# Kernel optimization log

Measured on AMD Instinct MI355X. Metric: run time of the kernel, lower is better.

## Reference

```python
import jax, jax.numpy as jnp
import numpy as np

B, L, H = 8192, 64, 128
DEPTH = 3
EPS = 1e-5


def setup_inputs() -> dict:
    key = jax.random.key(0)
    ks = jax.random.split(key, 1 + 6)
    hidden_states = jax.random.normal(ks[0], (B, L, H), dtype=jnp.float32)
    # stacked per-layer params: Linear(H,H) -> LayerNorm(H) -> ReLU -> Linear(H, H//2)
    s1 = 1.0 / np.sqrt(H)
    W1 = jax.random.uniform(ks[1], (DEPTH, H, H), jnp.float32, -s1, s1)
    b1 = jax.random.uniform(ks[2], (DEPTH, H), jnp.float32, -s1, s1)
    gamma = jnp.ones((DEPTH, H), jnp.float32)
    beta = jnp.zeros((DEPTH, H), jnp.float32)
    W2 = jax.random.uniform(ks[3], (DEPTH, H, H // 2), jnp.float32, -s1, s1)
    b2 = jax.random.uniform(ks[4], (DEPTH, H // 2), jnp.float32, -s1, s1)
    return {
        "hidden_states": hidden_states,
        "W1": W1, "b1": b1, "gamma": gamma, "beta": beta,
        "W2": W2, "b2": b2,
        "lengths": L,
    }


def _layernorm(x, g, b):
    mu = jnp.mean(x, axis=-1, keepdims=True)
    var = jnp.mean(jnp.square(x - mu), axis=-1, keepdims=True)
    return (x - mu) * jax.lax.rsqrt(var + EPS) * g + b


def reference(hidden_states, W1, b1, gamma, beta, W2, b2, lengths):
    # hidden_states: [B, L, H]; max(lengths) == L
    x = hidden_states
    for i in range(DEPTH):
        h = jnp.einsum('blh,hk->blk', x, W1[i]) + b1[i]          # [B, L, H]
        h = jax.nn.relu(_layernorm(h, gamma[i], beta[i]))
        x1 = jnp.einsum('blh,hk->blk', h, W2[i]) + b2[i]          # [B, L, H//2]
        x2 = jnp.max(x1, axis=1, keepdims=True)                   # max-pool over seq
        x2 = jnp.broadcast_to(x2, x1.shape)                       # repeat to L
        x = jnp.concatenate([x1, x2], axis=2)                     # [B, L, H]
    return jnp.max(x, axis=1)                                     # [B, H]
```

## Files before the change

### kernel.cpp

```cpp
#include <hip/hip_runtime.h>

#define NB 8192
#define NL 64
#define NH 128

typedef __bf16 bf16x8 __attribute__((ext_vector_type(8)));
typedef float f32x4 __attribute__((ext_vector_type(4)));
typedef float f32x2 __attribute__((ext_vector_type(2)));
typedef unsigned short ushort8 __attribute__((ext_vector_type(8)));

__device__ __host__ __forceinline__ int p2l(int p) {
  return (p & ~31) + ((p & 1) << 4) + ((p & 31) >> 1);
}
__device__ __host__ __forceinline__ int pi2(int p) {
  return (p & 1) ? 64 + (p >> 1) : (p >> 1);
}

__device__ __forceinline__ unsigned pk2(float lo, float hi) {
  union { __bf16 b[2]; unsigned u; } t;
  t.b[0] = (__bf16)lo; t.b[1] = (__bf16)hi;
  return t.u;
}

__global__ __launch_bounds__(256) void repack_w(const float* __restrict__ W1,
                                                const float* __restrict__ W2,
                                                const float* __restrict__ gamma,
                                                const float* __restrict__ beta,
                                                unsigned short* __restrict__ wp1,
                                                unsigned short* __restrict__ wp2,
                                                float* __restrict__ gbt) {
  int t = blockIdx.x * 256 + threadIdx.x;
  int lane = t & 63, g = t >> 6;
  if (g < 96) {
    int layer = g >> 5, rem = g & 31, nt = rem >> 2, ks = rem & 3;
    int n = nt * 16 + (lane & 15);
    int kb = ks * 32 + (lane >> 4) * 8;
    ushort8 v;
#pragma unroll
    for (int r = 0; r < 8; ++r) {
      int k = kb + r;
      int srck = (layer == 0) ? k : pi2(k);
      union { __bf16 b; unsigned short u; } c;
      c.b = (__bf16)W1[(layer * 128 + srck) * 128 + n];
      v[r] = c.u;
    }
    *reinterpret_cast<ushort8*>(wp1 + ((size_t)g * 64 + lane) * 8) = v;
  } else if (g < 144) {
    int g2 = g - 96;
    int layer = g2 >> 4, rem = g2 & 15, nt = rem >> 2, ks = rem & 3;
    int n = nt * 16 + (lane & 15);
    int kb = ks * 32 + (lane >> 4) * 8;
    ushort8 v;
#pragma unroll
    for (int r = 0; r < 8; ++r) {
      union { __bf16 b; unsigned short u; } c;
      c.b = (__bf16)W2[(layer * 128 + p2l(kb + r)) * 64 + n];
      v[r] = c.u;
    }
    *reinterpret_cast<ushort8*>(wp2 + ((size_t)g2 * 64 + lane) * 8) = v;
  } else if (g < 150) {
    int g2 = g - 144;
    int layer = g2 >> 1, param = g2 & 1;
    const float* src = (param == 0 ? gamma : beta) + layer * 128;
    float* dst = gbt + layer * 288 + param * 144;
    int p0 = lane * 2;
#pragma unroll
    for (int u = 0; u < 2; ++u) {
      int p = p0 + u;
      dst[(p >> 5) * 36 + (p & 31)] = src[p2l(p)];
    }
  }
}

__global__ __launch_bounds__(256) void fused_mlp(
    const float* __restrict__ hidden,
    const float* __restrict__ b1,
    const float* __restrict__ b2,
    const unsigned short* __restrict__ wp1u,
    const unsigned short* __restrict__ wp2u,
    const float* __restrict__ gbt,
    float* __restrict__ out) {
  __shared__ __align__(16) unsigned short xAu[NL * NH];
  __shared__ __align__(16) unsigned short xBu[NL * NH];
  __shared__ __align__(16) float gbuf[864];

  const int tid = threadIdx.x;
  const int wave = tid >> 6, lane = tid & 63;
  const int ci = lane & 15, lg = lane >> 4;
  char* xA = reinterpret_cast<char*>(xAu);
  char* xB = reinterpret_cast<char*>(xBu);

  const int abase = ci * 256;
  const int axor = ci << 4;

  if (tid < 96) {
#pragma unroll
    for (int u = 0; u < 9; ++u) gbuf[tid * 9 + u] = gbt[tid * 9 + u];
  }

  const float* src = hidden + (size_t)blockIdx.x * (NL * NH);
#pragma unroll
  for (int i = 0; i < 4; ++i) {
    int f = i * 256 + tid;
    int row = f >> 4;
    int cb = (f & 15) * 16;
    const float4* p = reinterpret_cast<const float4*>(src + f * 8);
    float4 a = p[0], bq = p[1];
    bf16x8 v;
    v[0] = (__bf16)a.x;  v[1] = (__bf16)a.y;  v[2] = (__bf16)a.z;  v[3] = (__bf16)a.w;
    v[4] = (__bf16)bq.x; v[5] = (__bf16)bq.y; v[6] = (__bf16)bq.z; v[7] = (__bf16)bq.w;
    *reinterpret_cast<bf16x8*>(xA + row * 256 + (cb ^ ((row & 15) << 4))) = v;
  }
  __syncthreads();

  for (int layer = 0; layer < 3; ++layer) {
    const unsigned short* wl1 = wp1u + (size_t)layer * 16384;
    const float bv0 = b1[layer * 128 + wave * 32 + ci];
    const float bv1 = b1[layer * 128 + wave * 32 + 16 + ci];
    const int dby = (wave * 16 + ci) * 4;

    f32x4 acc[4][2];
#pragma unroll
    for (int mt = 0; mt < 4; ++mt) {
      acc[mt][0] = f32x4{bv0, bv0, bv0, bv0};
      acc[mt][1] = f32x4{bv1, bv1, bv1, bv1};
    }
#pragma unroll
    for (int ks = 0; ks < 4; ++ks) {
      bf16x8 bf0 = *reinterpret_cast<const bf16x8*>(
          wl1 + (((wave * 2 + 0) * 4 + ks) * 64 + lane) * 8);
      bf16x8 bf1 = *reinterpret_cast<const bf16x8*>(
          wl1 + (((wave * 2 + 1) * 4 + ks) * 64 + lane) * 8);
      int cbx = ((ks * 64 + lg * 16) ^ axor) + abase;
#pragma unroll
      for (int mt = 0; mt < 4; ++mt) {
        bf16x8 af = *reinterpret_cast<const bf16x8*>(xA + mt * 4096 + cbx);
        acc[mt][0] = __builtin_amdgcn_mfma_f32_16x16x32_bf16(af, bf0, acc[mt][0], 0, 0, 0);
        acc[mt][1] = __builtin_amdgcn_mfma_f32_16x16x32_bf16(af, bf1, acc[mt][1], 0, 0, 0);
      }
    }
#pragma unroll
    for (int mt = 0; mt < 4; ++mt)
#pragma unroll
      for (int r = 0; r < 4; ++r) {
        int row = mt * 16 + lg * 4 + r;
        *reinterpret_cast<unsigned*>(
            xB + row * 256 + (dby ^ ((lg * 4 + r) << 4))) =
            pk2(acc[mt][0][r], acc[mt][1][r]);
      }
    __syncthreads();

    {
      const int row = wave * 16 + (lane >> 2);
      const int q = lane & 3;
      const int rb = row * 256, rx = (lane >> 2) << 4;
      bf16x8 h0 = *reinterpret_cast<const bf16x8*>(xB + rb + ((q * 64 + 0) ^ rx));
      bf16x8 h1 = *reinterpret_cast<const bf16x8*>(xB + rb + ((q * 64 + 16) ^ rx));
      bf16x8 h2 = *reinterpret_cast<const bf16x8*>(xB + rb + ((q * 64 + 32) ^ rx));
      bf16x8 h3 = *reinterpret_cast<const bf16x8*>(xB + rb + ((q * 64 + 48) ^ rx));
      f32x2 f[16];
#pragma unroll
      for (int cch = 0; cch < 4; ++cch) {
        bf16x8 hv = (cch == 0) ? h0 : (cch == 1) ? h1 : (cch == 2) ? h2 : h3;
#pragma unroll
        for (int j2 = 0; j2 < 4; ++j2)
          f[cch * 4 + j2] = f32x2{(float)hv[j2 * 2], (float)hv[j2 * 2 + 1]};
      }
      f32x2 s2 = {0.f, 0.f}, q2 = {0.f, 0.f};
#pragma unroll
      for (int i = 0; i < 16; ++i) { s2 += f[i]; q2 += f[i] * f[i]; }
      float s = s2.x + s2.y, sq = q2.x + q2.y;
      s += __shfl_xor(s, 1);  sq += __shfl_xor(sq, 1);
      s += __shfl_xor(s, 2);  sq += __shfl_xor(sq, 2);
      float mu = s * (1.f / 128.f);
      float var = sq * (1.f / 128.f) - mu * mu;
      float rs = rsqrtf(var + 1e-5f);
      const f32x2* gl = reinterpret_cast<const f32x2*>(gbuf + layer * 288 + q * 36);
      const f32x2* bl = reinterpret_cast<const f32x2*>(gbuf + layer * 288 + 144 + q * 36);
#pragma unroll
      for (int cch = 0; cch < 4; ++cch) {
        union { unsigned u[4]; bf16x8 v; } yy;
#pragma unroll
        for (int j2 = 0; j2 < 4; ++j2) {
          int i = cch * 4 + j2;
          f32x2 a2 = gl[i] * rs;
          f32x2 c2 = bl[i] - a2 * mu;
          f32x2 y2 = f[i] * a2 + c2;
          yy.u[j2] = pk2(fmaxf(y2.x, 0.f), fmaxf(y2.y, 0.f));
        }
        *reinterpret_cast<bf16x8*>(xB + rb + ((q * 64 + cch * 16) ^ rx)) = yy.v;
      }
    }
    __syncthreads();

    const unsigned short* wl2 = wp2u + (size_t)layer * 8192;
    f32x4 acc2[4];
    {
      float b2v = b2[layer * 64 + wave * 16 + ci];
#pragma unroll
      for (int mt = 0; mt < 4; ++mt) acc2[mt] = f32x4{b2v, b2v, b2v, b2v};
    }
#pragma unroll
    for (int ks = 0; ks < 4; ++ks) {
      bf16x8 bfr = *reinterpret_cast<const bf16x8*>(
          wl2 + ((wave * 4 + ks) * 64 + lane) * 8);
      int cbx = ((ks * 64 + lg * 16) ^ axor) + abase;
#pragma unroll
      for (int mt = 0; mt < 4; ++mt) {
        bf16x8 af = *reinterpret_cast<const bf16x8*>(xB + mt * 4096 + cbx);
        acc2[mt] = __builtin_amdgcn_mfma_f32_16x16x32_bf16(af, bfr, acc2[mt], 0, 0, 0);
      }
    }

    float mm;
    {
      float m = -3.0e38f;
#pragma unroll
      for (int mt = 0; mt < 4; ++mt)
#pragma unroll
        for (int r = 0; r < 4; ++r) m = fmaxf(m, acc2[mt][r]);
      m = fmaxf(m, __shfl_xor(m, 16));
      m = fmaxf(m, __shfl_xor(m, 32));
      mm = m;
    }

    if (layer < 2) {
#pragma unroll
      for (int mt = 0; mt < 4; ++mt)
#pragma unroll
        for (int r = 0; r < 4; ++r) {
          int row = mt * 16 + lg * 4 + r;
          *reinterpret_cast<unsigned*>(
              xA + row * 256 + (dby ^ ((lg * 4 + r) << 4))) =
              pk2(acc2[mt][r], mm);
        }
      __syncthreads();
    } else {
      if (lg == 0) {
        size_t o = (size_t)blockIdx.x * 128 + wave * 16 + ci;
        out[o] = mm;
        out[o + 64] = mm;
      }
    }
  }
}

extern "C" void kernel_launch(void* const* d_in, const int* in_sizes, int n_in,
                              void* d_out, int out_size, void* d_ws, size_t ws_size,
                              hipStream_t stream) {
  const float* hidden = (const float*)d_in[0];
  const float* W1 = (const float*)d_in[1];
  const float* b1 = (const float*)d_in[2];
  const float* gamma = (const float*)d_in[3];
  const float* beta = (const float*)d_in[4];
  const float* W2 = (const float*)d_in[5];
  const float* b2 = (const float*)d_in[6];
  (void)in_sizes; (void)n_in; (void)out_size; (void)ws_size;

  unsigned short* wp1 = (unsigned short*)d_ws;
  unsigned short* wp2 = wp1 + 3 * 8 * 4 * 64 * 8;
  float* gbt = (float*)(wp2 + 3 * 4 * 4 * 64 * 8);
  float* out = (float*)d_out;

  repack_w<<<38, 256, 0, stream>>>(W1, W2, gamma, beta, wp1, wp2, gbt);
  fused_mlp<<<NB, 256, 0, stream>>>(hidden, b1, b2, wp1, wp2, gbt, out);
}
```

Before: 144.1 us.

## Process two batch rows per block with software-pipelined interleaved stages

Each block now handles two sequences, using the two shared-memory buffers as per-sequence activations, and interleaves the GEMM, LayerNorm and pack stages of the two so one sequence's MFMA work overlaps the other's LDS and VALU work. The grid is halved. This aims to hide barrier stalls and the serial stage dependencies inside a single sequence, and to reuse the weight-fragment loads across two sequences. In exchange it raises register pressure from doubled accumulators, which may reduce occupancy, and leaves half as many blocks to fill the GPU.

```diff
diff --git a/kernel.cpp b/kernel.cpp
--- a/kernel.cpp
+++ b/kernel.cpp
@@ -92,34 +92,42 @@
 
   const int abase = ci * 256;
   const int axor = ci << 4;
+  const int dby = (wave * 16 + ci) * 4;
 
   if (tid < 96) {
 #pragma unroll
     for (int u = 0; u < 9; ++u) gbuf[tid * 9 + u] = gbt[tid * 9 + u];
   }
 
-  const float* src = hidden + (size_t)blockIdx.x * (NL * NH);
-#pragma unroll
-  for (int i = 0; i < 4; ++i) {
-    int f = i * 256 + tid;
-    int row = f >> 4;
-    int cb = (f & 15) * 16;
-    const float4* p = reinterpret_cast<const float4*>(src + f * 8);
-    float4 a = p[0], bq = p[1];
-    bf16x8 v;
-    v[0] = (__bf16)a.x;  v[1] = (__bf16)a.y;  v[2] = (__bf16)a.z;  v[3] = (__bf16)a.w;
-    v[4] = (__bf16)bq.x; v[5] = (__bf16)bq.y; v[6] = (__bf16)bq.z; v[7] = (__bf16)bq.w;
-    *reinterpret_cast<bf16x8*>(xA + row * 256 + (cb ^ ((row & 15) << 4))) = v;
+  {
+    const float* srcA = hidden + (size_t)(2 * blockIdx.x) * (NL * NH);
+#pragma unroll
+    for (int rr = 0; rr < 2; ++rr) {
+      const float* src = srcA + rr * (NL * NH);
+      char* xr = rr ? xB : xA;
+#pragma unroll
+      for (int i = 0; i < 4; ++i) {
+        int f = i * 256 + tid;
+        int row = f >> 4;
+        int cb = (f & 15) * 16;
+        const float4* p = reinterpret_cast<const float4*>(src + f * 8);
+        float4 a = p[0], bq = p[1];
+        bf16x8 v;
+        v[0] = (__bf16)a.x;  v[1] = (__bf16)a.y;  v[2] = (__bf16)a.z;  v[3] = (__bf16)a.w;
+        v[4] = (__bf16)bq.x; v[5] = (__bf16)bq.y; v[6] = (__bf16)bq.z; v[7] = (__bf16)bq.w;
+        *reinterpret_cast<bf16x8*>(xr + row * 256 + (cb ^ ((row & 15) << 4))) = v;
+      }
+    }
   }
   __syncthreads();
 
-  for (int layer = 0; layer < 3; ++layer) {
-    const unsigned short* wl1 = wp1u + (size_t)layer * 16384;
-    const float bv0 = b1[layer * 128 + wave * 32 + ci];
-    const float bv1 = b1[layer * 128 + wave * 32 + 16 + ci];
-    const int dby = (wave * 16 + ci) * 4;
-
-    f32x4 acc[4][2];
+  f32x4 accA[4][2], accB[4][2], acc2A[4], acc2B[4];
+  float mmA = 0.f, mmB = 0.f;
+
+  auto G1 = [&](const char* xR, f32x4 (&acc)[4][2], int l) {
+    const unsigned short* wl1 = wp1u + (size_t)l * 16384;
+    float bv0 = b1[l * 128 + wave * 32 + ci];
+    float bv1 = b1[l * 128 + wave * 32 + 16 + ci];
 #pragma unroll
     for (int mt = 0; mt < 4; ++mt) {
       acc[mt][0] = f32x4{bv0, bv0, bv0, bv0};
@@ -134,72 +142,72 @@
       int cbx = ((ks * 64 + lg * 16) ^ axor) + abase;
 #pragma unroll
       for (int mt = 0; mt < 4; ++mt) {
-        bf16x8 af = *reinterpret_cast<const bf16x8*>(xA + mt * 4096 + cbx);
+        bf16x8 af = *reinterpret_cast<const bf16x8*>(xR + mt * 4096 + cbx);
         acc[mt][0] = __builtin_amdgcn_mfma_f32_16x16x32_bf16(af, bf0, acc[mt][0], 0, 0, 0);
         acc[mt][1] = __builtin_amdgcn_mfma_f32_16x16x32_bf16(af, bf1, acc[mt][1], 0, 0, 0);
       }
     }
+  };
+
+  auto WH = [&](char* xR, f32x4 (&acc)[4][2]) {
 #pragma unroll
     for (int mt = 0; mt < 4; ++mt)
 #pragma unroll
       for (int r = 0; r < 4; ++r) {
         int row = mt * 16 + lg * 4 + r;
         *reinterpret_cast<unsigned*>(
-            xB + row * 256 + (dby ^ ((lg * 4 + r) << 4))) =
+            xR + row * 256 + (dby ^ ((lg * 4 + r) << 4))) =
             pk2(acc[mt][0][r], acc[mt][1][r]);
       }
-    __syncthreads();
-
-    {
-      const int row = wave * 16 + (lane >> 2);
-      const int q = lane & 3;
-      const int rb = row * 256, rx = (lane >> 2) << 4;
-      bf16x8 h0 = *reinterpret_cast<const bf16x8*>(xB + rb + ((q * 64 + 0) ^ rx));
-      bf16x8 h1 = *reinterpret_cast<const bf16x8*>(xB + rb + ((q * 64 + 16) ^ rx));
-      bf16x8 h2 = *reinterpret_cast<const bf16x8*>(xB + rb + ((q * 64 + 32) ^ rx));
-      bf16x8 h3 = *reinterpret_cast<const bf16x8*>(xB + rb + ((q * 64 + 48) ^ rx));
-      f32x2 f[16];
-#pragma unroll
-      for (int cch = 0; cch < 4; ++cch) {
-        bf16x8 hv = (cch == 0) ? h0 : (cch == 1) ? h1 : (cch == 2) ? h2 : h3;
-#pragma unroll
-        for (int j2 = 0; j2 < 4; ++j2)
-          f[cch * 4 + j2] = f32x2{(float)hv[j2 * 2], (float)hv[j2 * 2 + 1]};
-      }
-      f32x2 s2 = {0.f, 0.f}, q2 = {0.f, 0.f};
-#pragma unroll
-      for (int i = 0; i < 16; ++i) { s2 += f[i]; q2 += f[i] * f[i]; }
-      float s = s2.x + s2.y, sq = q2.x + q2.y;
-      s += __shfl_xor(s, 1);  sq += __shfl_xor(sq, 1);
-      s += __shfl_xor(s, 2);  sq += __shfl_xor(sq, 2);
-      float mu = s * (1.f / 128.f);
-      float var = sq * (1.f / 128.f) - mu * mu;
-      float rs = rsqrtf(var + 1e-5f);
-      const f32x2* gl = reinterpret_cast<const f32x2*>(gbuf + layer * 288 + q * 36);
-      const f32x2* bl = reinterpret_cast<const f32x2*>(gbuf + layer * 288 + 144 + q * 36);
-#pragma unroll
-      for (int cch = 0; cch < 4; ++cch) {
-        union { unsigned u[4]; bf16x8 v; } yy;
-#pragma unroll
-        for (int j2 = 0; j2 < 4; ++j2) {
-          int i = cch * 4 + j2;
-          f32x2 a2 = gl[i] * rs;
-          f32x2 c2 = bl[i] - a2 * mu;
-          f32x2 y2 = f[i] * a2 + c2;
-          yy.u[j2] = pk2(fmaxf(y2.x, 0.f), fmaxf(y2.y, 0.f));
-        }
-        *reinterpret_cast<bf16x8*>(xB + rb + ((q * 64 + cch * 16) ^ rx)) = yy.v;
-      }
-    }
-    __syncthreads();
-
-    const unsigned short* wl2 = wp2u + (size_t)layer * 8192;
-    f32x4 acc2[4];
-    {
-      float b2v = b2[layer * 64 + wave * 16 + ci];
-#pragma unroll
-      for (int mt = 0; mt < 4; ++mt) acc2[mt] = f32x4{b2v, b2v, b2v, b2v};
-    }
+  };
+
+  auto LN = [&](char* xR, int l) {
+    const int row = wave * 16 + (lane >> 2);
+    const int q = lane & 3;
+    const int rb = row * 256, rx = (lane >> 2) << 4;
+    bf16x8 h0 = *reinterpret_cast<const bf16x8*>(xR + rb + ((q * 64 + 0) ^ rx));
+    bf16x8 h1 = *reinterpret_cast<const bf16x8*>(xR + rb + ((q * 64 + 16) ^ rx));
+    bf16x8 h2 = *reinterpret_cast<const bf16x8*>(xR + rb + ((q * 64 + 32) ^ rx));
+    bf16x8 h3 = *reinterpret_cast<const bf16x8*>(xR + rb + ((q * 64 + 48) ^ rx));
+    f32x2 f[16];
+#pragma unroll
+    for (int cch = 0; cch < 4; ++cch) {
+      bf16x8 hv = (cch == 0) ? h0 : (cch == 1) ? h1 : (cch == 2) ? h2 : h3;
+#pragma unroll
+      for (int j2 = 0; j2 < 4; ++j2)
+        f[cch * 4 + j2] = f32x2{(float)hv[j2 * 2], (float)hv[j2 * 2 + 1]};
+    }
+    f32x2 s2 = {0.f, 0.f}, q2 = {0.f, 0.f};
+#pragma unroll
+    for (int i = 0; i < 16; ++i) { s2 += f[i]; q2 += f[i] * f[i]; }
+    float s = s2.x + s2.y, sq = q2.x + q2.y;
+    s += __shfl_xor(s, 1);  sq += __shfl_xor(sq, 1);
+    s += __shfl_xor(s, 2);  sq += __shfl_xor(sq, 2);
+    float mu = s * (1.f / 128.f);
+    float var = sq * (1.f / 128.f) - mu * mu;
+    float rs = rsqrtf(var + 1e-5f);
+    const f32x2* gl = reinterpret_cast<const f32x2*>(gbuf + l * 288 + q * 36);
+    const f32x2* bl = reinterpret_cast<const f32x2*>(gbuf + l * 288 + 144 + q * 36);
+#pragma unroll
+    for (int cch = 0; cch < 4; ++cch) {
+      union { unsigned u[4]; bf16x8 v; } yy;
+#pragma unroll
+      for (int j2 = 0; j2 < 4; ++j2) {
+        int i = cch * 4 + j2;
+        f32x2 a2 = gl[i] * rs;
+        f32x2 c2 = bl[i] - a2 * mu;
+        f32x2 y2 = f[i] * a2 + c2;
+        yy.u[j2] = pk2(fmaxf(y2.x, 0.f), fmaxf(y2.y, 0.f));
+      }
+      *reinterpret_cast<bf16x8*>(xR + rb + ((q * 64 + cch * 16) ^ rx)) = yy.v;
+    }
+  };
+
+  auto G2 = [&](const char* xR, f32x4 (&a2)[4], float& mm, int l) {
+    const unsigned short* wl2 = wp2u + (size_t)l * 8192;
+    float b2v = b2[l * 64 + wave * 16 + ci];
+#pragma unroll
+    for (int mt = 0; mt < 4; ++mt) a2[mt] = f32x4{b2v, b2v, b2v, b2v};
 #pragma unroll
     for (int ks = 0; ks < 4; ++ks) {
       bf16x8 bfr = *reinterpret_cast<const bf16x8*>(
@@ -207,42 +215,58 @@
       int cbx = ((ks * 64 + lg * 16) ^ axor) + abase;
 #pragma unroll
       for (int mt = 0; mt < 4; ++mt) {
-        bf16x8 af = *reinterpret_cast<const bf16x8*>(xB + mt * 4096 + cbx);
-        acc2[mt] = __builtin_amdgcn_mfma_f32_16x16x32_bf16(af, bfr, acc2[mt], 0, 0, 0);
-      }
-    }
-
-    float mm;
-    {
-      float m = -3.0e38f;
-#pragma unroll
-      for (int mt = 0; mt < 4; ++mt)
-#pragma unroll
-        for (int r = 0; r < 4; ++r) m = fmaxf(m, acc2[mt][r]);
-      m = fmaxf(m, __shfl_xor(m, 16));
-      m = fmaxf(m, __shfl_xor(m, 32));
-      mm = m;
-    }
-
-    if (layer < 2) {
-#pragma unroll
-      for (int mt = 0; mt < 4; ++mt)
-#pragma unroll
-        for (int r = 0; r < 4; ++r) {
-          int row = mt * 16 + lg * 4 + r;
-          *reinterpret_cast<unsigned*>(
-              xA + row * 256 + (dby ^ ((lg * 4 + r) << 4))) =
-              pk2(acc2[mt][r], mm);
-        }
-      __syncthreads();
-    } else {
-      if (lg == 0) {
-        size_t o = (size_t)blockIdx.x * 128 + wave * 16 + ci;
-        out[o] = mm;
-        out[o + 64] = mm;
-      }
-    }
-  }
+        bf16x8 af = *reinterpret_cast<const bf16x8*>(xR + mt * 4096 + cbx);
+        a2[mt] = __builtin_amdgcn_mfma_f32_16x16x32_bf16(af, bfr, a2[mt], 0, 0, 0);
+      }
+    }
+    float m = -3.0e38f;
+#pragma unroll
+    for (int mt = 0; mt < 4; ++mt)
+#pragma unroll
+      for (int r = 0; r < 4; ++r) m = fmaxf(m, a2[mt][r]);
+    m = fmaxf(m, __shfl_xor(m, 16));
+    m = fmaxf(m, __shfl_xor(m, 32));
+    mm = m;
+  };
+
+  auto PK = [&](char* xR, f32x4 (&a2)[4], float mm) {
+#pragma unroll
+    for (int mt = 0; mt < 4; ++mt)
+#pragma unroll
+      for (int r = 0; r < 4; ++r) {
+        int row = mt * 16 + lg * 4 + r;
+        *reinterpret_cast<unsigned*>(
+            xR + row * 256 + (dby ^ ((lg * 4 + r) << 4))) =
+            pk2(a2[mt][r], mm);
+      }
+  };
+
+  auto OUTW = [&](int rsel, float mm) {
+    if (lg == 0) {
+      size_t o = (size_t)(2 * blockIdx.x + rsel) * 128 + wave * 16 + ci;
+      out[o] = mm;
+      out[o + 64] = mm;
+    }
+  };
+
+  for (int l = 0; l < 3; ++l) {
+    G1(xA, accA, l);
+    if (l) PK(xB, acc2B, mmB);
+    __syncthreads();
+    WH(xA, accA);
+    G1(xB, accB, l);
+    __syncthreads();
+    LN(xA, l);
+    WH(xB, accB);
+    __syncthreads();
+    G2(xA, acc2A, mmA, l);
+    LN(xB, l);
+    __syncthreads();
+    if (l < 2) PK(xA, acc2A, mmA); else OUTW(0, mmA);
+    G2(xB, acc2B, mmB, l);
+    __syncthreads();
+  }
+  OUTW(1, mmB);
 }
 
 extern "C" void kernel_launch(void* const* d_in, const int* in_sizes, int n_in,
@@ -263,5 +287,5 @@
   float* out = (float*)d_out;
 
   repack_w<<<38, 256, 0, stream>>>(W1, W2, gamma, beta, wp1, wp2, gbt);
-  fused_mlp<<<NB, 256, 0, stream>>>(hidden, b1, b2, wp1, wp2, gbt, out);
-}
+  fused_mlp<<<NB / 2, 256, 0, stream>>>(hidden, b1, b2, wp1, wp2, gbt, out);
+}
```

New measurement: 163.9 us. 13.7% more time.
